# Kernel tuning notes

Measured on AMD Instinct MI355X. Metric: run time of the kernel, lower is better.

The kernel has to match this reference:

```python
import jax, jax.numpy as jnp
import numpy as np

N0, C1, C2 = 100000, 10000, 1000
E0 = 1_600_000
IN = 128
H = 128
OUT = 128


def _pool_edges(ei, ew, cluster, C):
    # PyG pool_edge: remap via cluster, drop self loops, coalesce (sum weights)
    m = cluster[ei]
    mask = m[0] != m[1]
    m = m[:, mask]
    w = ew[mask]
    keys = m[0] * C + m[1]
    uk, inv = np.unique(keys, return_inverse=True)
    w2 = np.bincount(inv, weights=w).astype(np.float32)
    return np.stack([uk // C, uk % C]).astype(np.int64), w2


def _with_self_loops(ei, ew, N):
    # gcn_norm(add_remaining_self_loops, fill_value=1); base edges have no loops
    row = np.concatenate([ei[0], np.arange(N)]).astype(np.int64)
    col = np.concatenate([ei[1], np.arange(N)]).astype(np.int64)
    w = np.concatenate([ew, np.ones(N, np.float32)])
    return row, col, w


def setup_inputs() -> dict:
    rng = np.random.default_rng(0)
    ei = rng.integers(0, N0, size=(2, E0))
    ei = ei[:, ei[0] != ei[1]]
    ew = np.ones(ei.shape[1], np.float32)
    # guaranteed-surjective cluster assignments (stand-in for Louvain output)
    c1 = rng.permutation(np.arange(N0) % C1).astype(np.int64)
    c2 = rng.permutation(np.arange(C1) % C2).astype(np.int64)
    ei1, ew1 = _pool_edges(ei, ew, c1, C1)
    ei2, ew2 = _pool_edges(ei1, ew1, c2, C2)
    r0, co0, w0 = _with_self_loops(ei, ew, N0)
    r1, co1, w1 = _with_self_loops(ei1, ew1, C1)
    r2, co2, w2 = _with_self_loops(ei2, ew2, C2)

    key = jax.random.key(0)
    ks = jax.random.split(key, 16)
    def lin(k, fi, fo):
        return jax.random.normal(k, (fi, fo), jnp.float32) / np.sqrt(fi)
    inp = {
        'x': jax.random.normal(ks[0], (N0, IN), jnp.float32),
        'W_pre': lin(ks[1], IN, H), 'b_pre': jnp.zeros((H,), jnp.float32),
        'W_u0': lin(ks[2], H, H), 'b_u0': jnp.zeros((H,), jnp.float32),
        'W_u1': lin(ks[3], H, H), 'b_u1': jnp.zeros((H,), jnp.float32),
        'W_u2': lin(ks[4], H, H), 'b_u2': jnp.zeros((H,), jnp.float32),
        'W_d0': lin(ks[5], H, OUT), 'b_d0': jnp.zeros((OUT,), jnp.float32),
        'W_d1': lin(ks[6], H, H), 'b_d1': jnp.zeros((H,), jnp.float32),
        'row0': jnp.asarray(r0), 'col0': jnp.asarray(co0), 'ew0': jnp.asarray(w0),
        'row1': jnp.asarray(r1), 'col1': jnp.asarray(co1), 'ew1': jnp.asarray(w1),
        'row2': jnp.asarray(r2), 'col2': jnp.asarray(co2), 'ew2': jnp.asarray(w2),
        'cluster1': jnp.asarray(c1), 'cluster2': jnp.asarray(c2),
    }
    return inp


def _gcn(x, W, b, row, col, ew, N):
    # PyG GCNConv: sym-normalized aggregation at target (col)
    deg = jax.ops.segment_sum(ew, col, num_segments=N)
    dinv = jnp.where(deg > 0, jax.lax.rsqrt(deg), 0.0)
    norm = dinv[row] * ew * dinv[col]
    h = x @ W                                   # [N, F_out]
    out = jax.ops.segment_sum(h[row] * norm[:, None], col, num_segments=N)
    return out + b


def _seg_mean(x, cluster, C):
    s = jax.ops.segment_sum(x, cluster, num_segments=C)
    cnt = jax.ops.segment_sum(jnp.ones((x.shape[0], 1), x.dtype), cluster,
                              num_segments=C)
    return s / jnp.maximum(cnt, 1.0)


def reference(x, W_pre, b_pre, W_u0, b_u0, W_u1, b_u1, W_u2, b_u2,
              W_d0, b_d0, W_d1, b_d1,
              row0, col0, ew0, row1, col1, ew1, row2, col2, ew2,
              cluster1, cluster2):
    # --- up (coarsening) path ---
    h = x @ W_pre + b_pre                                   # preembed
    x0 = jax.nn.relu(_gcn(h, W_u0, b_u0, row0, col0, ew0, N0))
    x1 = _seg_mean(x0, cluster1, C1)                        # avg_pool level 1
    x1 = jax.nn.relu(_gcn(x1, W_u1, b_u1, row1, col1, ew1, C1))
    x2 = _seg_mean(x1, cluster2, C2)                        # avg_pool level 2
    x2 = jax.nn.relu(_gcn(x2, W_u2, b_u2, row2, col2, ew2, C2))
    # --- down (unpooling) path; down convs use all-ones edge weights ---
    y = x1 + x2[cluster2]
    y = jax.nn.relu(_gcn(y, W_d1, b_d1, row1, col1, jnp.ones_like(ew1), C1))
    y = x0 + y[cluster1]
    y = _gcn(y, W_d0, b_d0, row0, col0, jnp.ones_like(ew0), N0)
    return y
```

## Files before the change

### kernel.cpp

```cpp
#include <hip/hip_runtime.h>

#define HH 128
static constexpr int kN0 = 100000;
static constexpr int kC1 = 10000;
static constexpr int kC2 = 1000;

static constexpr int B0 = kN0;
static constexpr int B1 = B0 + kC1;
static constexpr int B2 = B1 + kC2;
static constexpr int B3 = B2 + kC1;
static constexpr int NTOT = B3 + kC2;

static constexpr int NB0 = (kN0 + 127) / 128;
static constexpr int NB1 = (kC1 + 7) / 8;
static constexpr int NB2 = kC2;
static constexpr int NBP1 = (kC1 + 127) / 128;
static constexpr int NBP2 = (kC2 + 15) / 16;
static constexpr int Q0 = NB0;
static constexpr int Q1 = Q0 + NB1;
static constexpr int Q2 = Q1 + NB2;
static constexpr int Q3 = Q2 + NBP1;
static constexpr int NBK = Q3 + NBP2;

__device__ __forceinline__ int bucket_of(int bin) {
  if (bin < B0) return bin >> 7;
  if (bin < B1) return Q0 + ((bin - B0) >> 3);
  if (bin < B2) return Q1 + (bin - B1);
  if (bin < B3) return Q2 + ((bin - B2) >> 7);
  return Q3 + ((bin - B3) >> 4);
}

__device__ __forceinline__ unsigned int f2_to_bf2(float a, float b) {
  unsigned int ua = __float_as_uint(a);
  unsigned int ub = __float_as_uint(b);
  ua = (ua + 0x7fffu + ((ua >> 16) & 1u)) >> 16;
  ub = (ub + 0x7fffu + ((ub >> 16) & 1u)) & 0xffff0000u;
  return ua | ub;
}

__global__ __launch_bounds__(256) void p1_kernel(const int* __restrict__ col0,
                                                 const int* __restrict__ col1,
                                                 const int* __restrict__ col2,
                                                 const int* __restrict__ cl1,
                                                 const int* __restrict__ cl2,
                                                 int E0, int E1, int E2,
                                                 int* __restrict__ bucketCnt) {
  __shared__ int h[NBK];
  for (int i = threadIdx.x; i < NBK; i += 256) h[i] = 0;
  __syncthreads();
  int T0 = E0, T1 = T0 + E1, T2 = T1 + E2, T3 = T2 + kN0, T4 = T3 + kC1;
  for (int g = blockIdx.x * 256 + threadIdx.x; g < T4; g += gridDim.x * 256) {
    int bin;
    if (g < T0)      bin = col0[g];
    else if (g < T1) bin = B0 + col1[g - T0];
    else if (g < T2) bin = B1 + col2[g - T1];
    else if (g < T3) bin = B2 + cl1[g - T2];
    else             bin = B3 + cl2[g - T3];
    atomicAdd(&h[bucket_of(bin)], 1);
  }
  __syncthreads();
  for (int i = threadIdx.x; i < NBK; i += 256) {
    int c = h[i];
    if (c) atomicAdd(&bucketCnt[i], c);
  }
}

__global__ __launch_bounds__(1024) void p2_kernel(const int* __restrict__ bucketCnt,
                                                  int* __restrict__ bucketStart,
                                                  int* __restrict__ cursor,
                                                  int* __restrict__ startsg, int T) {
  int t = threadIdx.x;
  int v[4]; int s = 0;
#pragma unroll
  for (int j = 0; j < 4; j++) {
    int i = t * 4 + j;
    v[j] = (i < NBK) ? bucketCnt[i] : 0;
    s += v[j];
  }
  int lane = t & 63, w = t >> 6;
  int incl = s;
  for (int o = 1; o < 64; o <<= 1) { int u = __shfl_up(incl, o); if (lane >= o) incl += u; }
  __shared__ int wt[16];
  if (lane == 63) wt[w] = incl;
  __syncthreads();
  if (t == 0) { int run = 0; for (int i = 0; i < 16; i++) { int c = wt[i]; wt[i] = run; run += c; } }
  __syncthreads();
  int ex = wt[w] + incl - s;
#pragma unroll
  for (int j = 0; j < 4; j++) {
    int i = t * 4 + j;
    if (i < NBK) { bucketStart[i] = ex; cursor[i] = ex; }
    ex += v[j];
  }
  if (t == 0) { bucketStart[NBK] = T; startsg[NTOT] = T; }
}

__global__ __launch_bounds__(256) void p3_kernel(const int* __restrict__ col0,
                                                 const int* __restrict__ col1,
                                                 const int* __restrict__ col2,
                                                 const int* __restrict__ cl1,
                                                 const int* __restrict__ cl2,
                                                 const int* __restrict__ row0,
                                                 const int* __restrict__ row1,
                                                 const int* __restrict__ row2,
                                                 const float* __restrict__ ew1,
                                                 const float* __restrict__ ew2,
                                                 int E0, int E1, int E2,
                                                 int* __restrict__ cursor,
                                                 int4* __restrict__ part) {
  __shared__ int h[NBK];
  __shared__ int gbase[NBK];
  for (int i = threadIdx.x; i < NBK; i += 256) h[i] = 0;
  __syncthreads();
  int T0 = E0, T1 = T0 + E1, T2 = T1 + E2, T3 = T2 + kN0, T4 = T3 + kC1;
  int base = blockIdx.x * 4096;
  int bins[16], srcs[16], rk[16];
  float wv[16];
#pragma unroll
  for (int j = 0; j < 16; j++) {
    int g = base + threadIdx.x + j * 256;
    int bin = -1, src = 0; float w = 0.f;
    if (g < T4) {
      if (g < T0) { bin = col0[g]; src = row0[g]; }
      else if (g < T1) { int e = g - T0; bin = B0 + col1[e]; src = row1[e]; w = ew1[e]; }
      else if (g < T2) { int e = g - T1; bin = B1 + col2[e]; src = row2[e]; w = ew2[e]; }
      else if (g < T3) { int e = g - T2; bin = B2 + cl1[e]; src = e; }
      else             { int e = g - T3; bin = B3 + cl2[e]; src = e; }
    }
    bins[j] = bin; srcs[j] = src; wv[j] = w;
    rk[j] = (bin >= 0) ? atomicAdd(&h[bucket_of(bin)], 1) : 0;
  }
  __syncthreads();
  for (int i = threadIdx.x; i < NBK; i += 256) {
    int c = h[i];
    gbase[i] = c ? atomicAdd(&cursor[i], c) : 0;
  }
  __syncthreads();
#pragma unroll
  for (int j = 0; j < 16; j++) {
    if (bins[j] >= 0) {
      int slot = gbase[bucket_of(bins[j])] + rk[j];
      part[slot] = make_int4(bins[j], srcs[j], __float_as_int(wv[j]), 0);
    }
  }
}

__global__ __launch_bounds__(256) void p4_kernel(const int* __restrict__ bucketStart,
                                                 const int4* __restrict__ part,
                                                 int* __restrict__ startsg,
                                                 int* __restrict__ rowS,
                                                 float* __restrict__ ewSm) {
  int b = blockIdx.x;
  int binLo, width;
  if (b < Q0)      { binLo = b << 7;                 width = 128; if (binLo + width > B0) width = B0 - binLo; }
  else if (b < Q1) { binLo = B0 + ((b - Q0) << 3);   width = 8; }
  else if (b < Q2) { binLo = B1 + (b - Q1);          width = 1; }
  else if (b < Q3) { binLo = B2 + ((b - Q2) << 7);   width = 128; if (binLo + width > B3) width = B3 - binLo; }
  else             { binLo = B3 + ((b - Q3) << 4);   width = 16; if (binLo + width > NTOT) width = NTOT - binLo; }
  int base = bucketStart[b], nend = bucketStart[b + 1];
  int t = threadIdx.x;

  if (width == 1) {
    if (t == 0) startsg[binLo] = base;
    bool isEw = (binLo >= B0 && binLo < B2);
    for (int i = base + t; i < nend; i += 256) {
      int4 it = part[i];
      rowS[i] = it.y;
      if (isEw) ewSm[i] = __int_as_float(it.z);
    }
    return;
  }

  __shared__ int h[128];
  __shared__ int cur[128];
  if (t < 128) h[t] = 0;
  __syncthreads();
  for (int i = base + t; i < nend; i += 256) atomicAdd(&h[part[i].x - binLo], 1);
  __syncthreads();
  if (t == 0) {
    int run = 0;
    for (int j = 0; j < width; j++) {
      cur[j] = run;
      startsg[binLo + j] = base + run;
      run += h[j];
    }
  }
  __syncthreads();
  for (int i = base + t; i < nend; i += 256) {
    int4 it = part[i];
    int k = it.x;
    int r = atomicAdd(&cur[k - binLo], 1);
    int dst = base + r;
    rowS[dst] = it.y;
    if (k >= B0 && k < B2) ewSm[dst] = __int_as_float(it.z);
  }
}

__global__ void dinv_kernel(const int* __restrict__ startsg, const float* __restrict__ ewSm,
                            float* __restrict__ d0, float* __restrict__ d1w,
                            float* __restrict__ d1o, float* __restrict__ d2) {
  int t = blockIdx.x * 256 + threadIdx.x;
  if (t < kN0) {
    int c = startsg[t + 1] - startsg[t];
    d0[t] = c > 0 ? rsqrtf((float)c) : 0.f;
  }
  int wid = t >> 6, lane = t & 63;
  if (wid < kC1) {
    int s = startsg[B0 + wid], e = startsg[B0 + wid + 1];
    float a = 0.f;
    for (int k = s + lane; k < e; k += 64) a += ewSm[k];
    for (int o = 32; o > 0; o >>= 1) a += __shfl_down(a, o);
    if (lane == 0) {
      d1w[wid] = a > 0.f ? rsqrtf(a) : 0.f;
      int c = e - s;
      d1o[wid] = c > 0 ? rsqrtf((float)c) : 0.f;
    }
  } else if (wid < kC1 + kC2) {
    int w2 = wid - kC1;
    int s = startsg[B1 + w2], e = startsg[B1 + w2 + 1];
    float a = 0.f;
    for (int k = s + lane; k < e; k += 64) a += ewSm[k];
    for (int o = 32; o > 0; o >>= 1) a += __shfl_down(a, o);
    if (lane == 0) d2[w2] = a > 0.f ? rsqrtf(a) : 0.f;
  }
}

__global__ void wprep_kernel(const int* __restrict__ rowS, const float* __restrict__ ewSm,
                             const float* __restrict__ dinv0, const float* __restrict__ d1w,
                             const float* __restrict__ d1o, const float* __restrict__ d2,
                             int E0, int E1, int E2,
                             float* __restrict__ wAll, float* __restrict__ w1om) {
  int e = blockIdx.x * 256 + threadIdx.x;
  int tot = E0 + E1 + E2;
  if (e >= tot) return;
  int r = rowS[e];
  if (e < E0) {
    wAll[e] = dinv0[r];
  } else if (e < E0 + E1) {
    wAll[e] = d1w[r] * ewSm[e];
    w1om[e] = d1o[r];
  } else {
    wAll[e] = d2[r] * ewSm[e];
  }
}

__global__ __launch_bounds__(256) void matmul_kernel(const float* __restrict__ X,
                                                     const float* __restrict__ Xadd,
                                                     const int* __restrict__ cl,
                                                     const float* __restrict__ W,
                                                     const float* __restrict__ bias,
                                                     float* __restrict__ Y,
                                                     unsigned int* __restrict__ Ybf, int N) {
  __shared__ float Ws[64 * 128];
  __shared__ float Xs[32 * 128];
  int t = threadIdx.x;
  int rbase = blockIdx.x * 32;
  const float4* X4 = (const float4*)X;
  float4* Xs4 = (float4*)Xs;
#pragma unroll
  for (int i = 0; i < 4; i++) {
    int idx = t + 256 * i;
    int fr = idx >> 5, fc = idx & 31;
    int row = rbase + fr; if (row >= N) row = N - 1;
    float4 v = X4[(size_t)row * 32 + fc];
    if (Xadd) {
      int c = cl[row];
      float4 u = ((const float4*)Xadd)[(size_t)c * 32 + fc];
      v.x += u.x; v.y += u.y; v.z += u.z; v.w += u.w;
    }
    Xs4[idx] = v;
  }
  float acc[4][4];
#pragma unroll
  for (int r = 0; r < 4; r++)
#pragma unroll
    for (int cc = 0; cc < 4; cc++) acc[r][cc] = 0.f;
  int c0 = (t & 31) * 4;
  int rl = (t >> 5) * 4;
  const float4* W4 = (const float4*)W;
  float4* Ws4 = (float4*)Ws;
  for (int half = 0; half < 2; half++) {
    __syncthreads();
#pragma unroll
    for (int i = 0; i < 8; i++) {
      int idx = t + 256 * i;
      Ws4[idx] = W4[half * 2048 + idx];
    }
    __syncthreads();
#pragma unroll 4
    for (int k = 0; k < 64; k++) {
      float4 w4 = *(const float4*)(Ws + k * 128 + c0);
      float xv[4];
#pragma unroll
      for (int r = 0; r < 4; r++) xv[r] = Xs[(rl + r) * 128 + half * 64 + k];
#pragma unroll
      for (int r = 0; r < 4; r++) {
        acc[r][0] = fmaf(xv[r], w4.x, acc[r][0]);
        acc[r][1] = fmaf(xv[r], w4.y, acc[r][1]);
        acc[r][2] = fmaf(xv[r], w4.z, acc[r][2]);
        acc[r][3] = fmaf(xv[r], w4.w, acc[r][3]);
      }
    }
  }
  float4 b4 = make_float4(0.f, 0.f, 0.f, 0.f);
  if (bias) b4 = *(const float4*)(bias + c0);
#pragma unroll
  for (int r = 0; r < 4; r++) {
    int row = rbase + rl + r;
    if (row < N) {
      float4 o;
      o.x = acc[r][0] + b4.x; o.y = acc[r][1] + b4.y;
      o.z = acc[r][2] + b4.z; o.w = acc[r][3] + b4.w;
      if (Ybf) {
        unsigned int pk0 = f2_to_bf2(o.x, o.y);
        unsigned int pk1 = f2_to_bf2(o.z, o.w);
        *(uint2*)(Ybf + (size_t)row * 64 + (c0 >> 1)) = make_uint2(pk0, pk1);
      } else {
        *(float4*)(Y + (size_t)row * 128 + c0) = o;
      }
    }
  }
}

__global__ __launch_bounds__(256) void agg_kernel(const unsigned int* __restrict__ Hf,
                                                  float* __restrict__ out,
                                                  const int* __restrict__ starts,
                                                  const int* __restrict__ rowS,
                                                  const float* __restrict__ wS,
                                                  const float* __restrict__ dinv,
                                                  const float* __restrict__ bias,
                                                  int C, int relu) {
  int wid = (blockIdx.x * blockDim.x + threadIdx.x) >> 6;
  int lane = threadIdx.x & 63;
  if (wid >= C) return;
  int s = starts[wid], e = starts[wid + 1];
  float dc = dinv[wid];
  float ax[4] = {0.f, 0.f, 0.f, 0.f}, ay[4] = {0.f, 0.f, 0.f, 0.f};
  for (int base = s; base < e; base += 64) {
    int n = e - base; if (n > 64) n = 64;
    int moff = base + (lane < n ? lane : 0);
    int r = rowS[moff];
    float w = wS[moff];
    int j = 0;
    for (; j + 7 < n; j += 8) {
#pragma unroll
      for (int u = 0; u < 8; u++) {
        int rr = __shfl(r, j + u);
        float ww = __shfl(w, j + u);
        unsigned int pv = Hf[(size_t)rr * 64 + lane];
        ax[u & 3] = fmaf(ww, __uint_as_float(pv << 16), ax[u & 3]);
        ay[u & 3] = fmaf(ww, __uint_as_float(pv & 0xffff0000u), ay[u & 3]);
      }
    }
    for (; j < n; j++) {
      int rr = __shfl(r, j);
      float ww = __shfl(w, j);
      unsigned int pv = Hf[(size_t)rr * 64 + lane];
      ax[0] = fmaf(ww, __uint_as_float(pv << 16), ax[0]);
      ay[0] = fmaf(ww, __uint_as_float(pv & 0xffff0000u), ay[0]);
    }
  }
  float ox = (ax[0] + ax[1] + ax[2] + ax[3]) * dc + bias[lane * 2];
  float oy = (ay[0] + ay[1] + ay[2] + ay[3]) * dc + bias[lane * 2 + 1];
  if (relu) { ox = fmaxf(ox, 0.f); oy = fmaxf(oy, 0.f); }
  *(float2*)(out + (size_t)wid * 128 + lane * 2) = make_float2(ox, oy);
}

__global__ __launch_bounds__(256) void aggb_kernel(const unsigned int* __restrict__ Hf,
                                                   float* __restrict__ out,
                                                   const int* __restrict__ starts,
                                                   const int* __restrict__ rowS,
                                                   const float* __restrict__ wS,
                                                   const float* __restrict__ dinv,
                                                   const float* __restrict__ bias,
                                                   int C, int relu) {
  int node = blockIdx.x;
  if (node >= C) return;
  int wv = threadIdx.x >> 6, lane = threadIdx.x & 63;
  int s = starts[node], e = starts[node + 1];
  float ax[4] = {0.f, 0.f, 0.f, 0.f}, ay[4] = {0.f, 0.f, 0.f, 0.f};
  for (int base = s + wv * 64; base < e; base += 256) {
    int n = e - base; if (n > 64) n = 64;
    int moff = base + (lane < n ? lane : 0);
    int r = rowS[moff];
    float w = wS[moff];
    int j = 0;
    for (; j + 7 < n; j += 8) {
#pragma unroll
      for (int u = 0; u < 8; u++) {
        int rr = __shfl(r, j + u);
        float ww = __shfl(w, j + u);
        unsigned int pv = Hf[(size_t)rr * 64 + lane];
        ax[u & 3] = fmaf(ww, __uint_as_float(pv << 16), ax[u & 3]);
        ay[u & 3] = fmaf(ww, __uint_as_float(pv & 0xffff0000u), ay[u & 3]);
      }
    }
    for (; j < n; j++) {
      int rr = __shfl(r, j);
      float ww = __shfl(w, j);
      unsigned int pv = Hf[(size_t)rr * 64 + lane];
      ax[0] = fmaf(ww, __uint_as_float(pv << 16), ax[0]);
      ay[0] = fmaf(ww, __uint_as_float(pv & 0xffff0000u), ay[0]);
    }
  }
  __shared__ float shx[256], shy[256];
  shx[threadIdx.x] = ax[0] + ax[1] + ax[2] + ax[3];
  shy[threadIdx.x] = ay[0] + ay[1] + ay[2] + ay[3];
  __syncthreads();
  if (threadIdx.x < 64) {
    float sx = shx[lane] + shx[lane + 64] + shx[lane + 128] + shx[lane + 192];
    float sy = shy[lane] + shy[lane + 64] + shy[lane + 128] + shy[lane + 192];
    float dc = dinv[node];
    float ox = sx * dc + bias[lane * 2];
    float oy = sy * dc + bias[lane * 2 + 1];
    if (relu) { ox = fmaxf(ox, 0.f); oy = fmaxf(oy, 0.f); }
    *(float2*)(out + (size_t)node * 128 + lane * 2) = make_float2(ox, oy);
  }
}

__global__ __launch_bounds__(256) void pool_kernel(const float* __restrict__ src,
                                                   float* __restrict__ out,
                                                   const int* __restrict__ starts,
                                                   const int* __restrict__ rowS, int C) {
  int wid = (blockIdx.x * blockDim.x + threadIdx.x) >> 6;
  int lane = threadIdx.x & 63;
  if (wid >= C) return;
  int s = starts[wid], e = starts[wid + 1];
  float ax0 = 0.f, ay0 = 0.f, ax1 = 0.f, ay1 = 0.f;
  int m = s;
  for (; m + 3 < e; m += 4) {
    int i0 = rowS[m], i1 = rowS[m + 1], i2 = rowS[m + 2], i3 = rowS[m + 3];
    float2 v0 = *(const float2*)(src + (size_t)i0 * 128 + lane * 2);
    float2 v1 = *(const float2*)(src + (size_t)i1 * 128 + lane * 2);
    float2 v2 = *(const float2*)(src + (size_t)i2 * 128 + lane * 2);
    float2 v3 = *(const float2*)(src + (size_t)i3 * 128 + lane * 2);
    ax0 += v0.x; ay0 += v0.y;
    ax1 += v1.x; ay1 += v1.y;
    ax0 += v2.x; ay0 += v2.y;
    ax1 += v3.x; ay1 += v3.y;
  }
  for (; m < e; m++) {
    int id = rowS[m];
    const float2 v = *(const float2*)(src + (size_t)id * 128 + lane * 2);
    ax0 += v.x; ay0 += v.y;
  }
  float inv = (e > s) ? 1.f / (float)(e - s) : 0.f;
  *(float2*)(out + (size_t)wid * 128 + lane * 2) =
      make_float2((ax0 + ax1) * inv, (ay0 + ay1) * inv);
}

__global__ void addgather_kernel(const float* __restrict__ a, const float* __restrict__ b,
                                 const int* __restrict__ cl, float* __restrict__ out, int nrows) {
  int g = blockIdx.x * 256 + threadIdx.x;
  if (g >= nrows * 32) return;
  int rowi = g >> 5;
  int c = cl[rowi];
  float4 va = ((const float4*)a)[g];
  float4 vb = ((const float4*)b)[(size_t)c * 32 + (g & 31)];
  float4 o;
  o.x = va.x + vb.x; o.y = va.y + vb.y; o.z = va.z + vb.z; o.w = va.w + vb.w;
  ((float4*)out)[g] = o;
}


extern "C" void kernel_launch(void* const* d_in, const int* in_sizes, int n_in,
                              void* d_out, int out_size, void* d_ws, size_t ws_size,
                              hipStream_t stream) {
  const float* x     = (const float*)d_in[0];
  const float* W_pre = (const float*)d_in[1];
  const float* b_pre = (const float*)d_in[2];
  const float* W_u0  = (const float*)d_in[3];
  const float* b_u0  = (const float*)d_in[4];
  const float* W_u1  = (const float*)d_in[5];
  const float* b_u1  = (const float*)d_in[6];
  const float* W_u2  = (const float*)d_in[7];
  const float* b_u2  = (const float*)d_in[8];
  const float* W_d0  = (const float*)d_in[9];
  const float* b_d0  = (const float*)d_in[10];
  const float* W_d1  = (const float*)d_in[11];
  const float* b_d1  = (const float*)d_in[12];
  const int* row0 = (const int*)d_in[13];
  const int* col0 = (const int*)d_in[14];
  const int* row1 = (const int*)d_in[16];
  const int* col1 = (const int*)d_in[17];
  const float* ew1 = (const float*)d_in[18];
  const int* row2 = (const int*)d_in[19];
  const int* col2 = (const int*)d_in[20];
  const float* ew2 = (const float*)d_in[21];
  const int* cluster1 = (const int*)d_in[22];
  const int* cluster2 = (const int*)d_in[23];
  int E0 = in_sizes[13], E1 = in_sizes[16], E2 = in_sizes[19];
  float* out = (float*)d_out;
  int Ttot = E0 + E1 + E2 + kN0 + kC1;
  int Etot = E0 + E1 + E2;

  char* basep = (char*)d_ws;
  size_t off = 0;
  auto alloc = [&](size_t bytes) -> char* {
    char* p = basep + off;
    off = (off + bytes + 255) & ~(size_t)255;
    return p;
  };
  int* bucketCnt = (int*)alloc((size_t)NBK * 4);
  size_t zero_bytes = off;
  int* bucketStart = (int*)alloc((size_t)(NBK + 1) * 4);
  int* cursor      = (int*)alloc((size_t)NBK * 4);
  int* startsg     = (int*)alloc((size_t)(NTOT + 1) * 4);
  int* rowS  = (int*)alloc((size_t)Ttot * 4);
  float* ewS = (float*)alloc((size_t)(E1 + E2) * 4);
  float* ewSm = ewS - E0;
  float* dinv0  = (float*)alloc((size_t)kN0 * 4);
  float* dinv1w = (float*)alloc((size_t)kC1 * 4);
  float* dinv1o = (float*)alloc((size_t)kC1 * 4);
  float* dinv2  = (float*)alloc((size_t)kC2 * 4);
  size_t watermark = off;
  int4* part = (int4*)alloc((size_t)Ttot * 16);
  off = watermark;
  float* wAll = (float*)alloc((size_t)Etot * 4);
  float* w1o  = (float*)alloc((size_t)E1 * 4);
  float* w1om = w1o - E0;
  float* A    = (float*)alloc((size_t)kN0 * HH * 4);
  float* s1a  = (float*)alloc((size_t)kC1 * HH * 4);
  float* s1b  = (float*)alloc((size_t)kC1 * HH * 4);
  float* s2a  = (float*)alloc((size_t)kC2 * HH * 4);
  unsigned int* s1bb = (unsigned int*)alloc((size_t)kC1 * 64 * 4);
  unsigned int* s2bb = (unsigned int*)alloc((size_t)kC2 * 64 * 4);
  unsigned int* s1cb = (unsigned int*)alloc((size_t)kC1 * 64 * 4);
  unsigned int* tb   = (unsigned int*)alloc((size_t)kN0 * 64 * 4);
  unsigned int* t0   = (unsigned int*)d_out;

  hipMemsetAsync(d_ws, 0, zero_bytes, stream);

  auto cdiv = [](int a, int b) { return (a + b - 1) / b; };

  p1_kernel<<<256, 256, 0, stream>>>(col0, col1, col2, cluster1, cluster2, E0, E1, E2, bucketCnt);
  p2_kernel<<<1, 1024, 0, stream>>>(bucketCnt, bucketStart, cursor, startsg, Ttot);
  p3_kernel<<<cdiv(Ttot, 4096), 256, 0, stream>>>(col0, col1, col2, cluster1, cluster2,
                                                  row0, row1, row2, ew1, ew2, E0, E1, E2,
                                                  cursor, part);
  p4_kernel<<<NBK, 256, 0, stream>>>(bucketStart, part, startsg, rowS, ewSm);
  dinv_kernel<<<cdiv((kC1 + kC2) * 64, 256), 256, 0, stream>>>(startsg, ewSm, dinv0, dinv1w,
                                                               dinv1o, dinv2);
  wprep_kernel<<<cdiv(Etot, 256), 256, 0, stream>>>(rowS, ewSm, dinv0, dinv1w, dinv1o, dinv2,
                                                    E0, E1, E2, wAll, w1om);

  matmul_kernel<<<cdiv(kN0, 32), 256, 0, stream>>>(x, nullptr, nullptr, W_pre, b_pre, A, nullptr, kN0);
  matmul_kernel<<<cdiv(kN0, 32), 256, 0, stream>>>(A, nullptr, nullptr, W_u0, nullptr, nullptr, t0, kN0);
  agg_kernel<<<cdiv(kN0, 4), 256, 0, stream>>>(t0, A, startsg, rowS, wAll, dinv0, b_u0, kN0, 1);
  pool_kernel<<<cdiv(kC1, 4), 256, 0, stream>>>(A, s1a, startsg + B2, rowS, kC1);
  matmul_kernel<<<cdiv(kC1, 32), 256, 0, stream>>>(s1a, nullptr, nullptr, W_u1, nullptr, nullptr, s1bb, kC1);
  aggb_kernel<<<kC1, 256, 0, stream>>>(s1bb, s1a, startsg + B0, rowS, wAll, dinv1w, b_u1, kC1, 1);
  pool_kernel<<<cdiv(kC2, 4), 256, 0, stream>>>(s1a, s2a, startsg + B3, rowS, kC2);
  matmul_kernel<<<cdiv(kC2, 32), 256, 0, stream>>>(s2a, nullptr, nullptr, W_u2, nullptr, nullptr, s2bb, kC2);
  aggb_kernel<<<kC2, 256, 0, stream>>>(s2bb, s2a, startsg + B1, rowS, wAll, dinv2, b_u2, kC2, 1);
  matmul_kernel<<<cdiv(kC1, 32), 256, 0, stream>>>(s1a, s2a, cluster2, W_d1, nullptr, nullptr, s1cb, kC1);
  aggb_kernel<<<kC1, 256, 0, stream>>>(s1cb, s1b, startsg + B0, rowS, w1om, dinv1o, b_d1, kC1, 1);
  addgather_kernel<<<cdiv(kN0 * 32, 256), 256, 0, stream>>>(A, s1b, cluster1, A, kN0);
  matmul_kernel<<<cdiv(kN0, 32), 256, 0, stream>>>(A, nullptr, nullptr, W_d0, nullptr, nullptr, tb, kN0);
  agg_kernel<<<cdiv(kN0, 4), 256, 0, stream>>>(tb, out, startsg, rowS, wAll, dinv0, b_d0, kN0, 0);
}
```

Baseline: 774.6 us.

## Fold preembed into first GCN weight and fuse unpool add into matmul

Precomputes W_pre@W_u0 and b_pre@W_u0 so the first level needs one N0x128x128 matmul instead of two, and skips writing the intermediate A. The separate addgather kernel is removed: the final down matmul now gathers s1b by cluster1 and adds it to A while loading its input. This cuts a full-size matmul pass and a 100k-row read/write round trip. The fused weight changes floating-point rounding slightly.

Measured after the change: 708.7 us. 1.09x faster.

```diff
diff --git a/kernel.cpp b/kernel.cpp
--- a/kernel.cpp
+++ b/kernel.cpp
@@ -447,19 +447,6 @@
   float inv = (e > s) ? 1.f / (float)(e - s) : 0.f;
   *(float2*)(out + (size_t)wid * 128 + lane * 2) =
       make_float2((ax0 + ax1) * inv, (ay0 + ay1) * inv);
-}
-
-__global__ void addgather_kernel(const float* __restrict__ a, const float* __restrict__ b,
-                                 const int* __restrict__ cl, float* __restrict__ out, int nrows) {
-  int g = blockIdx.x * 256 + threadIdx.x;
-  if (g >= nrows * 32) return;
-  int rowi = g >> 5;
-  int c = cl[rowi];
-  float4 va = ((const float4*)a)[g];
-  float4 vb = ((const float4*)b)[(size_t)c * 32 + (g & 31)];
-  float4 o;
-  o.x = va.x + vb.x; o.y = va.y + vb.y; o.z = va.z + vb.z; o.w = va.w + vb.w;
-  ((float4*)out)[g] = o;
 }
 
 
@@ -519,6 +506,8 @@
   float* wAll = (float*)alloc((size_t)Etot * 4);
   float* w1o  = (float*)alloc((size_t)E1 * 4);
   float* w1om = w1o - E0;
+  float* Wf   = (float*)alloc((size_t)128 * 128 * 4);
+  float* bfv  = (float*)alloc((size_t)128 * 4);
   float* A    = (float*)alloc((size_t)kN0 * HH * 4);
   float* s1a  = (float*)alloc((size_t)kC1 * HH * 4);
   float* s1b  = (float*)alloc((size_t)kC1 * HH * 4);
@@ -544,18 +533,25 @@
   wprep_kernel<<<cdiv(Etot, 256), 256, 0, stream>>>(rowS, ewSm, dinv0, dinv1w, dinv1o, dinv2,
                                                     E0, E1, E2, wAll, w1om);
 
-  matmul_kernel<<<cdiv(kN0, 32), 256, 0, stream>>>(x, nullptr, nullptr, W_pre, b_pre, A, nullptr, kN0);
-  matmul_kernel<<<cdiv(kN0, 32), 256, 0, stream>>>(A, nullptr, nullptr, W_u0, nullptr, nullptr, t0, kN0);
+  matmul_kernel<<<cdiv(128, 32), 256, 0, stream>>>(W_pre, nullptr, nullptr, W_u0, nullptr,
+                                                   Wf, nullptr, 128);
+  matmul_kernel<<<1, 256, 0, stream>>>(b_pre, nullptr, nullptr, W_u0, nullptr,
+                                       bfv, nullptr, 1);
+  matmul_kernel<<<cdiv(kN0, 32), 256, 0, stream>>>(x, nullptr, nullptr, Wf, bfv,
+                                                   nullptr, t0, kN0);
   agg_kernel<<<cdiv(kN0, 4), 256, 0, stream>>>(t0, A, startsg, rowS, wAll, dinv0, b_u0, kN0, 1);
   pool_kernel<<<cdiv(kC1, 4), 256, 0, stream>>>(A, s1a, startsg + B2, rowS, kC1);
-  matmul_kernel<<<cdiv(kC1, 32), 256, 0, stream>>>(s1a, nullptr, nullptr, W_u1, nullptr, nullptr, s1bb, kC1);
+  matmul_kernel<<<cdiv(kC1, 32), 256, 0, stream>>>(s1a, nullptr, nullptr, W_u1, nullptr,
+                                                   nullptr, s1bb, kC1);
   aggb_kernel<<<kC1, 256, 0, stream>>>(s1bb, s1a, startsg + B0, rowS, wAll, dinv1w, b_u1, kC1, 1);
   pool_kernel<<<cdiv(kC2, 4), 256, 0, stream>>>(s1a, s2a, startsg + B3, rowS, kC2);
-  matmul_kernel<<<cdiv(kC2, 32), 256, 0, stream>>>(s2a, nullptr, nullptr, W_u2, nullptr, nullptr, s2bb, kC2);
+  matmul_kernel<<<cdiv(kC2, 32), 256, 0, stream>>>(s2a, nullptr, nullptr, W_u2, nullptr,
+                                                   nullptr, s2bb, kC2);
   aggb_kernel<<<kC2, 256, 0, stream>>>(s2bb, s2a, startsg + B1, rowS, wAll, dinv2, b_u2, kC2, 1);
-  matmul_kernel<<<cdiv(kC1, 32), 256, 0, stream>>>(s1a, s2a, cluster2, W_d1, nullptr, nullptr, s1cb, kC1);
+  matmul_kernel<<<cdiv(kC1, 32), 256, 0, stream>>>(s1a, s2a, cluster2, W_d1, nullptr,
+                                                   nullptr, s1cb, kC1);
   aggb_kernel<<<kC1, 256, 0, stream>>>(s1cb, s1b, startsg + B0, rowS, w1om, dinv1o, b_d1, kC1, 1);
-  addgather_kernel<<<cdiv(kN0 * 32, 256), 256, 0, stream>>>(A, s1b, cluster1, A, kN0);
-  matmul_kernel<<<cdiv(kN0, 32), 256, 0, stream>>>(A, nullptr, nullptr, W_d0, nullptr, nullptr, tb, kN0);
+  matmul_kernel<<<cdiv(kN0, 32), 256, 0, stream>>>(A, s1b, cluster1, W_d0, nullptr,
+                                                   nullptr, tb, kN0);
   agg_kernel<<<cdiv(kN0, 4), 256, 0, stream>>>(tb, out, startsg, rowS, wAll, dinv0, b_d0, kN0, 0);
 }
```
